# Optimization experiments

Measured on AMD Instinct MI355X. Metric: run time of the kernel, lower is better.

The kernel has to match this reference:

```python
import jax, jax.numpy as jnp
import numpy as np

D_MODEL = 1024
N_HEADS = 16
D_K = D_MODEL // N_HEADS
D_FF = 4096
LN_EPS = 1e-5


def _layer_norm(x, gamma, beta):
    mu = jnp.mean(x, axis=-1, keepdims=True)
    var = jnp.mean(jnp.square(x - mu), axis=-1, keepdims=True)
    return (x - mu) * jax.lax.rsqrt(var + LN_EPS) * gamma + beta


def setup_inputs() -> dict:
    key = jax.random.key(0)
    ks = jax.random.split(key, 16)
    B, S = 2, 2048
    x = jax.random.normal(ks[0], (B, S, D_MODEL), dtype=jnp.float32)
    # causal mask: True = masked (as used by masked_fill)
    mask = ~jnp.tril(jnp.ones((S, S), dtype=bool))
    s = 1.0 / np.sqrt(D_MODEL)
    sf = 1.0 / np.sqrt(D_FF)
    inp = {
        "x": x,
        "mask": mask,
        "ln1_g": jnp.ones((D_MODEL,), jnp.float32),
        "ln1_b": jnp.zeros((D_MODEL,), jnp.float32),
        "ln2_g": jnp.ones((D_MODEL,), jnp.float32),
        "ln2_b": jnp.zeros((D_MODEL,), jnp.float32),
        "Wq": jax.random.normal(ks[1], (D_MODEL, D_MODEL), jnp.float32) * s,
        "bq": jax.random.normal(ks[2], (D_MODEL,), jnp.float32) * s,
        "Wk": jax.random.normal(ks[3], (D_MODEL, D_MODEL), jnp.float32) * s,
        "bk": jax.random.normal(ks[4], (D_MODEL,), jnp.float32) * s,
        "Wv": jax.random.normal(ks[5], (D_MODEL, D_MODEL), jnp.float32) * s,
        "bv": jax.random.normal(ks[6], (D_MODEL,), jnp.float32) * s,
        "Wo": jax.random.normal(ks[7], (D_MODEL, D_MODEL), jnp.float32) * s,
        "bo": jax.random.normal(ks[8], (D_MODEL,), jnp.float32) * s,
        "W1": jax.random.normal(ks[9], (D_MODEL, D_FF), jnp.float32) * s,
        "b1": jax.random.normal(ks[10], (D_FF,), jnp.float32) * s,
        "W2": jax.random.normal(ks[11], (D_FF, D_MODEL), jnp.float32) * sf,
        "b2": jax.random.normal(ks[12], (D_MODEL,), jnp.float32) * sf,
    }
    return inp


def reference(x, mask, ln1_g, ln1_b, ln2_g, ln2_b,
              Wq, bq, Wk, bk, Wv, bv, Wo, bo, W1, b1, W2, b2):
    B, S, _ = x.shape
    normed = _layer_norm(x, ln1_g, ln1_b)
    # project and split heads: [B, H, S, Dk]
    def split_heads(t):
        return t.reshape(B, S, N_HEADS, D_K).transpose(0, 2, 1, 3)
    Q = split_heads(normed @ Wq + bq)
    K = split_heads(normed @ Wk + bk)
    V = split_heads(normed @ Wv + bv)
    qk = jnp.einsum("bhsd,bhtd->bhst", Q, K)  # [B, H, S, S]
    qk = jnp.where(mask, -jnp.inf, qk)  # mask applied BEFORE scaling, as in source
    attn = jax.nn.softmax(qk / np.sqrt(D_K), axis=-1)
    attn_out = jnp.einsum("bhst,bhtd->bhsd", attn, V)
    attn_out = attn_out.transpose(0, 2, 1, 3).reshape(B, S, D_MODEL)
    attn_out = attn_out @ Wo + bo
    res = attn_out + x  # dropout_p=0 (eval)
    h = _layer_norm(res, ln2_g, ln2_b)
    h = jax.nn.gelu(h @ W1 + b1, approximate=False)
    h = h @ W2 + b2
    return res + h
```

## Files before the change

kernel.cpp:

```cpp
#include <hip/hip_runtime.h>


typedef __bf16 bf16;
typedef __bf16 bf16x4 __attribute__((ext_vector_type(4)));
typedef __bf16 bf16x8 __attribute__((ext_vector_type(8)));
typedef float f32x4 __attribute__((ext_vector_type(4)));

#define NROWS 4096
#define DM 1024
#define SEQ 2048
#define NHEAD 16
#define DKH 64
#define DFF 4096
#define QSCALE 0.18033688f

#define GLL16(gptr, lptr) \
  __builtin_amdgcn_global_load_lds((const __attribute__((address_space(1))) void*)(gptr), \
                                   (__attribute__((address_space(3))) void*)(lptr), 16, 0, 0)

static char* g_scratch = nullptr;
namespace {
struct ScratchInit {
  ScratchInit() {
    void* p = nullptr;
    if (hipMalloc(&p, (size_t)128 * 1024 * 1024) == hipSuccess) g_scratch = (char*)p;
  }
};
static ScratchInit g_scratch_init;
}

__device__ inline unsigned cvt_pk_bf16(float lo, float hi) {
  unsigned r;
  asm("v_cvt_pk_bf16_f32 %0, %1, %2" : "=v"(r) : "v"(lo), "v"(hi));
  return r;
}

__global__ __launch_bounds__(256) void ln_kernel(const float* __restrict__ inp,
                                                 const float* __restrict__ gamma,
                                                 const float* __restrict__ beta,
                                                 bf16* __restrict__ out) {
  int row = blockIdx.x;
  int t = threadIdx.x;
  float4 xv = *((const float4*)(inp + (size_t)row * DM) + t);
  float v[4] = {xv.x, xv.y, xv.z, xv.w};
  float s = 0.f, sq = 0.f;
#pragma unroll
  for (int i = 0; i < 4; i++) { s += v[i]; sq += v[i] * v[i]; }
#pragma unroll
  for (int m = 32; m >= 1; m >>= 1) { s += __shfl_xor(s, m); sq += __shfl_xor(sq, m); }
  __shared__ float rs[4], rq[4];
  int w = t >> 6, lane = t & 63;
  if (lane == 0) { rs[w] = s; rq[w] = sq; }
  __syncthreads();
  s = rs[0] + rs[1] + rs[2] + rs[3];
  sq = rq[0] + rq[1] + rq[2] + rq[3];
  float mu = s * (1.f / DM);
  float var = sq * (1.f / DM) - mu * mu;
  float rinv = rsqrtf(var + 1e-5f);
  float4 gv = *((const float4*)gamma + t);
  float4 bv = *((const float4*)beta + t);
  float g[4] = {gv.x, gv.y, gv.z, gv.w}, b[4] = {bv.x, bv.y, bv.z, bv.w};
  bf16 ov[4];
#pragma unroll
  for (int i = 0; i < 4; i++) ov[i] = (bf16)((v[i] - mu) * rinv * g[i] + b[i]);
  *(uint2*)(out + (size_t)row * DM + t * 4) = *(uint2*)ov;
}

__global__ __launch_bounds__(256) void concat_bias(const float* __restrict__ bq,
                                                   const float* __restrict__ bk,
                                                   const float* __restrict__ bv,
                                                   float* __restrict__ cat) {
  int i = blockIdx.x * 256 + threadIdx.x;
  float v = (i < 1024) ? bq[i] : (i < 2048 ? bk[i - 1024] : bv[i - 2048]);
  cat[i] = v;
}

__global__ __launch_bounds__(1024) void transpose_f32_bf16(const float* __restrict__ in,
                                                           bf16* __restrict__ out,
                                                           int R, int C) {
  __shared__ bf16 tile[32][33];
  int x = blockIdx.x * 32 + threadIdx.x;
  int y = blockIdx.y * 32 + threadIdx.y;
  tile[threadIdx.y][threadIdx.x] = (bf16)in[(size_t)y * C + x];
  __syncthreads();
  int ox = blockIdx.y * 32 + threadIdx.x;
  int oy = blockIdx.x * 32 + threadIdx.y;
  out[(size_t)oy * R + ox] = tile[threadIdx.x][threadIdx.y];
}

__global__ __launch_bounds__(1024) void transpose_bf16(const bf16* __restrict__ in,
                                                       bf16* __restrict__ out,
                                                       int R, int C) {
  __shared__ bf16 tile[32][33];
  size_t zoff = (size_t)blockIdx.z * (size_t)R * (size_t)C;
  int x = blockIdx.x * 32 + threadIdx.x;
  int y = blockIdx.y * 32 + threadIdx.y;
  tile[threadIdx.y][threadIdx.x] = in[zoff + (size_t)y * C + x];
  __syncthreads();
  int ox = blockIdx.y * 32 + threadIdx.x;
  int oy = blockIdx.x * 32 + threadIdx.y;
  out[zoff + (size_t)oy * R + ox] = tile[threadIdx.x][threadIdx.y];
}

#define BM 128
#define BK 64

#define EPI_QKV3 0
#define EPI_ATTN_RES 1
#define EPI_GELU 2
#define EPI_FFN2 3

template<int EPI, int BNT>
__global__ __launch_bounds__(256, 2) void gemm_bt(
    const bf16* __restrict__ A, const bf16* __restrict__ Bt,
    const float* __restrict__ bias, int Kd, int N,
    bf16* __restrict__ outb, float* __restrict__ outf,
    const float* __restrict__ add) {
  constexpr int MS = (BNT == 128) ? 4 : 2;
  __shared__ bf16 As[BM * BK];
  __shared__ bf16 Bs[BNT * BK];
  int t = threadIdx.x;
  int m0 = blockIdx.y * BM, n0 = blockIdx.x * BNT;
  int w = t >> 6, lane = t & 63, ln = lane & 15, quad = lane >> 4;
  int wm = (BNT == 128) ? (w >> 1) * 64 : w * 32;
  int wn = (BNT == 128) ? (w & 1) * 64 : 0;
  f32x4 acc[MS][4];
#pragma unroll
  for (int i = 0; i < MS; i++)
#pragma unroll
    for (int j = 0; j < 4; j++) acc[i][j] = (f32x4){0.f, 0.f, 0.f, 0.f};

  int lr = (t >> 3) & 7, lc = t & 7;
  int gcol = ((lc ^ lr) * 8);
  const bf16* Ab = A + (size_t)(m0 + w * 8 + lr) * Kd + gcol;
  const bf16* Bb = Bt + (size_t)(n0 + w * 8 + lr) * Kd + gcol;
  bf16* AsW = As + (w * 8) * BK;
  bf16* BsW = Bs + (w * 8) * BK;

  for (int k0 = 0; k0 < Kd; k0 += BK) {
    __syncthreads();
#pragma unroll
    for (int j = 0; j < 4; j++)
      GLL16(Ab + (size_t)(32 * j) * Kd + k0, AsW + 32 * j * BK);
#pragma unroll
    for (int j = 0; j < BNT / 32; j++)
      GLL16(Bb + (size_t)(32 * j) * Kd + k0, BsW + 32 * j * BK);
    __syncthreads();
#pragma unroll
    for (int kk = 0; kk < 2; kk++) {
      bf16x8 af[MS], bfr[4];
#pragma unroll
      for (int ms = 0; ms < MS; ms++) {
        int r = wm + ms * 16 + ln;
        af[ms] = *(const bf16x8*)(As + r * BK + (((kk * 4 + quad) ^ (r & 7)) * 8));
      }
#pragma unroll
      for (int ns = 0; ns < 4; ns++) {
        int r = wn + ns * 16 + ln;
        bfr[ns] = *(const bf16x8*)(Bs + r * BK + (((kk * 4 + quad) ^ (r & 7)) * 8));
      }
#pragma unroll
      for (int ms = 0; ms < MS; ms++)
#pragma unroll
        for (int ns = 0; ns < 4; ns++)
          acc[ms][ns] = __builtin_amdgcn_mfma_f32_16x16x32_bf16(af[ms], bfr[ns], acc[ms][ns], 0, 0, 0);
    }
  }

#pragma unroll
  for (int ms = 0; ms < MS; ms++) {
#pragma unroll
    for (int ns = 0; ns < 4; ns++) {
      int col = n0 + wn + ns * 16 + ln;
      float bv = bias[col];
#pragma unroll
      for (int r = 0; r < 4; r++) {
        int row = m0 + wm + ms * 16 + quad * 4 + r;
        float val = acc[ms][ns][r] + bv;
        if (EPI == EPI_QKV3) {
          int which = col >> 10, cc = col & 1023;
          int h = cc >> 6, dk = cc & 63;
          float sc = (which == 0) ? QSCALE : 1.f;
          int b = row >> 11, sx = row & 2047;
          outb[(size_t)which * (4 << 20) +
               ((((size_t)b * NHEAD + h) * SEQ) + sx) * DKH + dk] = (bf16)(val * sc);
        } else if (EPI == EPI_ATTN_RES) {
          size_t idx = (size_t)row * DM + col;
          outf[idx] = val + add[idx];
        } else if (EPI == EPI_GELU) {
          float gl = 0.5f * val * (1.f + erff(val * 0.7071067811865475f));
          outb[(size_t)row * N + col] = (bf16)gl;
        } else {
          size_t idx = (size_t)row * DM + col;
          outf[idx] = val + add[idx];
        }
      }
    }
  }
}

#define OSTR 68

__global__ __launch_bounds__(256) void attn_kernel(
    const bf16* __restrict__ Q, const bf16* __restrict__ K,
    const bf16* __restrict__ Vt, bf16* __restrict__ out) {
  __shared__ float smem[2 * 32 * OSTR + 128];
  int lin = blockIdx.x;
  int bh = lin & 31;
  int qq = 63 - (lin >> 5);
  int t = threadIdx.x, w = t >> 6, lane = t & 63, ln = lane & 15, quad = lane >> 4;
  int qbase = qq * 32;
  size_t bhS = (size_t)bh * SEQ;
  const bf16* Vg0 = Vt + (size_t)bh * DKH * SEQ;

  bf16x8 qa[2][2];
#pragma unroll
  for (int m = 0; m < 2; m++)
#pragma unroll
    for (int ks = 0; ks < 2; ks++)
      qa[m][ks] = *(const bf16x8*)(Q + (bhS + qbase + m * 16 + ln) * DKH + ks * 32 + quad * 8);

  bf16x8 ones;
#pragma unroll
  for (int i = 0; i < 8; i++) ones[i] = (bf16)1.0f;

  f32x4 o[2][4];
#pragma unroll
  for (int m = 0; m < 2; m++)
#pragma unroll
    for (int i = 0; i < 4; i++) o[m][i] = (f32x4){0.f, 0.f, 0.f, 0.f};
  f32x4 accl[2] = {(f32x4){0.f, 0.f, 0.f, 0.f}, (f32x4){0.f, 0.f, 0.f, 0.f}};

  int ktmax = qq >> 1;
  for (int kt = w; kt <= ktmax; kt += 4) {
    const bf16* Kg = K + (bhS + kt * 64) * DKH;
    bf16x8 kbf[8], vbf[8];
#pragma unroll
    for (int ns = 0; ns < 4; ns++)
#pragma unroll
      for (int ks = 0; ks < 2; ks++)
        kbf[ns * 2 + ks] = *(const bf16x8*)(Kg + (ns * 16 + ln) * DKH + ks * 32 + quad * 8);
#pragma unroll
    for (int ns = 0; ns < 4; ns++)
#pragma unroll
      for (int j = 0; j < 2; j++) {
        const bf16* vrow = Vg0 + (size_t)(ns * 16 + ln) * SEQ + kt * 64 + j * 32 + quad * 4;
        union { bf16x8 v; bf16x4 h[2]; } tmp;
        tmp.h[0] = *(const bf16x4*)(vrow);
        tmp.h[1] = *(const bf16x4*)(vrow + 16);
        vbf[ns * 2 + j] = tmp.v;
      }

    f32x4 s[2][4];
#pragma unroll
    for (int m = 0; m < 2; m++)
#pragma unroll
      for (int ns = 0; ns < 4; ns++) s[m][ns] = (f32x4){0.f, 0.f, 0.f, 0.f};
#pragma unroll
    for (int ns = 0; ns < 4; ns++)
#pragma unroll
      for (int m = 0; m < 2; m++) {
        s[m][ns] = __builtin_amdgcn_mfma_f32_16x16x32_bf16(kbf[ns * 2], qa[m][0], s[m][ns], 0, 0, 0);
        s[m][ns] = __builtin_amdgcn_mfma_f32_16x16x32_bf16(kbf[ns * 2 + 1], qa[m][1], s[m][ns], 0, 0, 0);
      }
    if (kt == ktmax) {
#pragma unroll
      for (int m = 0; m < 2; m++)
#pragma unroll
        for (int ns = 0; ns < 4; ns++)
#pragma unroll
          for (int r = 0; r < 4; r++) {
            int qrow = qbase + m * 16 + ln;
            int kpos = kt * 64 + ns * 16 + quad * 4 + r;
            if (kpos > qrow) s[m][ns][r] = -30000.f;
          }
    }
#pragma unroll
    for (int m = 0; m < 2; m++)
#pragma unroll
      for (int ns = 0; ns < 4; ns++)
#pragma unroll
        for (int r = 0; r < 4; r++)
          s[m][ns][r] = __builtin_amdgcn_exp2f(s[m][ns][r]);
    bf16x8 pa[2][2];
#pragma unroll
    for (int m = 0; m < 2; m++)
#pragma unroll
      for (int j = 0; j < 2; j++) {
        union { bf16x8 v; unsigned u[4]; } pk;
        pk.u[0] = cvt_pk_bf16(s[m][2 * j][0], s[m][2 * j][1]);
        pk.u[1] = cvt_pk_bf16(s[m][2 * j][2], s[m][2 * j][3]);
        pk.u[2] = cvt_pk_bf16(s[m][2 * j + 1][0], s[m][2 * j + 1][1]);
        pk.u[3] = cvt_pk_bf16(s[m][2 * j + 1][2], s[m][2 * j + 1][3]);
        pa[m][j] = pk.v;
      }
#pragma unroll
    for (int m = 0; m < 2; m++) {
      accl[m] = __builtin_amdgcn_mfma_f32_16x16x32_bf16(pa[m][0], ones, accl[m], 0, 0, 0);
      accl[m] = __builtin_amdgcn_mfma_f32_16x16x32_bf16(pa[m][1], ones, accl[m], 0, 0, 0);
    }
#pragma unroll
    for (int ns2 = 0; ns2 < 4; ns2++)
#pragma unroll
      for (int m = 0; m < 2; m++) {
        o[m][ns2] = __builtin_amdgcn_mfma_f32_16x16x32_bf16(pa[m][0], vbf[ns2 * 2], o[m][ns2], 0, 0, 0);
        o[m][ns2] = __builtin_amdgcn_mfma_f32_16x16x32_bf16(pa[m][1], vbf[ns2 * 2 + 1], o[m][ns2], 0, 0, 0);
      }
  }

  float* Ob = smem;
  float* Lb = smem + 2 * 32 * OSTR;
#pragma unroll
  for (int m = 0; m < 2; m++) {
    if (w < 2) {
#pragma unroll
      for (int ns2 = 0; ns2 < 4; ns2++)
#pragma unroll
        for (int r = 0; r < 4; r++)
          Ob[(w * 32 + m * 16 + quad * 4 + r) * OSTR + ns2 * 16 + ln] = o[m][ns2][r];
    }
    if (ln == 0) {
#pragma unroll
      for (int r = 0; r < 4; r++) Lb[w * 32 + m * 16 + quad * 4 + r] = accl[m][r];
    }
  }
  __syncthreads();
  if (w >= 2) {
#pragma unroll
    for (int m = 0; m < 2; m++)
#pragma unroll
      for (int ns2 = 0; ns2 < 4; ns2++)
#pragma unroll
        for (int r = 0; r < 4; r++) {
          int idx = ((w - 2) * 32 + m * 16 + quad * 4 + r) * OSTR + ns2 * 16 + ln;
          Ob[idx] += o[m][ns2][r];
        }
  }
  __syncthreads();

  int r = t >> 3, c0 = (t & 7) * 8;
  float l = Lb[r] + Lb[32 + r] + Lb[64 + r] + Lb[96 + r];
  float inv = 1.f / l;
  bf16 ov[8];
#pragma unroll
  for (int j = 0; j < 8; j++) {
    float v = Ob[r * OSTR + c0 + j] + Ob[(32 + r) * OSTR + c0 + j];
    ov[j] = (bf16)(v * inv);
  }
  int b = bh >> 4, h = bh & 15;
  *(uint4*)(out + ((size_t)b * SEQ + qbase + r) * DM + h * DKH + c0) = *(uint4*)ov;
}

extern "C" void kernel_launch(void* const* d_in, const int* in_sizes, int n_in,
                              void* d_out, int out_size, void* d_ws, size_t ws_size,
                              hipStream_t stream) {
  const float* x    = (const float*)d_in[0];
  const float* ln1g = (const float*)d_in[2];
  const float* ln1b = (const float*)d_in[3];
  const float* ln2g = (const float*)d_in[4];
  const float* ln2b = (const float*)d_in[5];
  const float* Wq = (const float*)d_in[6];   const float* bq = (const float*)d_in[7];
  const float* Wk = (const float*)d_in[8];   const float* bk = (const float*)d_in[9];
  const float* Wv = (const float*)d_in[10];  const float* bv = (const float*)d_in[11];
  const float* Wo = (const float*)d_in[12];  const float* bo = (const float*)d_in[13];
  const float* W1 = (const float*)d_in[14];  const float* b1 = (const float*)d_in[15];
  const float* W2 = (const float*)d_in[16];  const float* b2 = (const float*)d_in[17];
  float* outp = (float*)d_out;

  char* scratch = g_scratch ? g_scratch : (char*)d_ws;

  bf16* Wqt = (bf16*)scratch;
  bf16* Wkt = Wqt + (1 << 20);
  bf16* Wvt = Wkt + (1 << 20);
  bf16* Wot = Wvt + (1 << 20);
  bf16* W1t = Wot + (1 << 20);
  bf16* W2t = W1t + (4 << 20);
  bf16* normed = W2t + (4 << 20);
  bf16* Qb = normed + (4 << 20);
  bf16* Kb = Qb + (4 << 20);
  bf16* Vb = Kb + (4 << 20);
  bf16* Vtb = Vb + (4 << 20);
  bf16* attn_o = Vtb + (4 << 20);
  float* resf = (float*)(attn_o + (4 << 20));
  float* bias_cat = resf + (4 << 20);
  bf16* h1 = Qb;

  dim3 b256(256), b1k(32, 32);

  ln_kernel<<<NROWS, b256, 0, stream>>>(x, ln1g, ln1b, normed);
  concat_bias<<<12, b256, 0, stream>>>(bq, bk, bv, bias_cat);

  transpose_f32_bf16<<<dim3(32, 32), b1k, 0, stream>>>(Wq, Wqt, 1024, 1024);
  transpose_f32_bf16<<<dim3(32, 32), b1k, 0, stream>>>(Wk, Wkt, 1024, 1024);
  transpose_f32_bf16<<<dim3(32, 32), b1k, 0, stream>>>(Wv, Wvt, 1024, 1024);
  transpose_f32_bf16<<<dim3(32, 32), b1k, 0, stream>>>(Wo, Wot, 1024, 1024);
  transpose_f32_bf16<<<dim3(128, 32), b1k, 0, stream>>>(W1, W1t, 1024, 4096);
  transpose_f32_bf16<<<dim3(32, 128), b1k, 0, stream>>>(W2, W2t, 4096, 1024);

  gemm_bt<EPI_QKV3, 128><<<dim3(24, 32), b256, 0, stream>>>(
      normed, Wqt, bias_cat, 1024, 3072, Qb, nullptr, nullptr);

  transpose_bf16<<<dim3(2, 64, 32), b1k, 0, stream>>>(Vb, Vtb, 2048, 64);

  attn_kernel<<<dim3(2048), b256, 0, stream>>>(Qb, Kb, Vtb, attn_o);

  gemm_bt<EPI_ATTN_RES, 64><<<dim3(16, 32), b256, 0, stream>>>(
      attn_o, Wot, bo, 1024, 1024, nullptr, resf, x);

  ln_kernel<<<NROWS, b256, 0, stream>>>(resf, ln2g, ln2b, normed);

  gemm_bt<EPI_GELU, 128><<<dim3(32, 32), b256, 0, stream>>>(
      normed, W1t, b1, 1024, 4096, h1, nullptr, nullptr);

  gemm_bt<EPI_FFN2, 64><<<dim3(16, 32), b256, 0, stream>>>(
      h1, W2t, b2, 4096, 1024, nullptr, outp, resf);
}
```

Before: 426.5 us.

## Prefetch next K tile in attention loop and permute V transpose for 16-byte loads

The attention loop is restructured to double-buffer K fragments in registers, loading the next K tile while computing the current one. Separately, the V transpose kernel writes columns in a permuted order so each lane can fetch its V fragment with one 16-byte load instead of two 8-byte loads. This targets global load latency and instruction count in the attention kernel. The cost is higher register pressure, which could lower occupancy.

```diff
diff --git a/kernel.cpp b/kernel.cpp
--- a/kernel.cpp
+++ b/kernel.cpp
@@ -2,7 +2,6 @@
 
 
 typedef __bf16 bf16;
-typedef __bf16 bf16x4 __attribute__((ext_vector_type(4)));
 typedef __bf16 bf16x8 __attribute__((ext_vector_type(8)));
 typedef float f32x4 __attribute__((ext_vector_type(4)));
 
@@ -88,9 +87,9 @@
   out[(size_t)oy * R + ox] = tile[threadIdx.x][threadIdx.y];
 }
 
-__global__ __launch_bounds__(1024) void transpose_bf16(const bf16* __restrict__ in,
-                                                       bf16* __restrict__ out,
-                                                       int R, int C) {
+__global__ __launch_bounds__(1024) void transpose_bf16_vperm(const bf16* __restrict__ in,
+                                                             bf16* __restrict__ out,
+                                                             int R, int C) {
   __shared__ bf16 tile[32][33];
   size_t zoff = (size_t)blockIdx.z * (size_t)R * (size_t)C;
   int x = blockIdx.x * 32 + threadIdx.x;
@@ -99,7 +98,8 @@
   __syncthreads();
   int ox = blockIdx.y * 32 + threadIdx.x;
   int oy = blockIdx.x * 32 + threadIdx.y;
-  out[zoff + (size_t)oy * R + ox] = tile[threadIdx.x][threadIdx.y];
+  int oxp = (ox & ~31) | (((ox >> 2) & 3) << 3) | (((ox >> 4) & 1) << 2) | (ox & 3);
+  out[zoff + (size_t)oy * R + oxp] = tile[threadIdx.x][threadIdx.y];
 }
 
 #define BM 128
@@ -232,25 +232,23 @@
   f32x4 accl[2] = {(f32x4){0.f, 0.f, 0.f, 0.f}, (f32x4){0.f, 0.f, 0.f, 0.f}};
 
   int ktmax = qq >> 1;
-  for (int kt = w; kt <= ktmax; kt += 4) {
-    const bf16* Kg = K + (bhS + kt * 64) * DKH;
-    bf16x8 kbf[8], vbf[8];
+
+  auto LOADK = [&](bf16x8 (&kf)[8], int kt_) {
+    const bf16* Kg = K + (bhS + kt_ * 64) * DKH;
 #pragma unroll
     for (int ns = 0; ns < 4; ns++)
 #pragma unroll
       for (int ks = 0; ks < 2; ks++)
-        kbf[ns * 2 + ks] = *(const bf16x8*)(Kg + (ns * 16 + ln) * DKH + ks * 32 + quad * 8);
+        kf[ns * 2 + ks] = *(const bf16x8*)(Kg + (ns * 16 + ln) * DKH + ks * 32 + quad * 8);
+  };
+  auto LOADV = [&](bf16x8 (&vf)[8], int kt_) {
 #pragma unroll
     for (int ns = 0; ns < 4; ns++)
 #pragma unroll
-      for (int j = 0; j < 2; j++) {
-        const bf16* vrow = Vg0 + (size_t)(ns * 16 + ln) * SEQ + kt * 64 + j * 32 + quad * 4;
-        union { bf16x8 v; bf16x4 h[2]; } tmp;
-        tmp.h[0] = *(const bf16x4*)(vrow);
-        tmp.h[1] = *(const bf16x4*)(vrow + 16);
-        vbf[ns * 2 + j] = tmp.v;
-      }
-
+      for (int ks = 0; ks < 2; ks++)
+        vf[ns * 2 + ks] = *(const bf16x8*)(Vg0 + (size_t)(ns * 16 + ln) * SEQ + kt_ * 64 + ks * 32 + quad * 8);
+  };
+  auto COMPUTE = [&](bf16x8 (&kf)[8], bf16x8 (&vf)[8], int kt_) {
     f32x4 s[2][4];
 #pragma unroll
     for (int m = 0; m < 2; m++)
@@ -260,10 +258,10 @@
     for (int ns = 0; ns < 4; ns++)
 #pragma unroll
       for (int m = 0; m < 2; m++) {
-        s[m][ns] = __builtin_amdgcn_mfma_f32_16x16x32_bf16(kbf[ns * 2], qa[m][0], s[m][ns], 0, 0, 0);
-        s[m][ns] = __builtin_amdgcn_mfma_f32_16x16x32_bf16(kbf[ns * 2 + 1], qa[m][1], s[m][ns], 0, 0, 0);
-      }
-    if (kt == ktmax) {
+        s[m][ns] = __builtin_amdgcn_mfma_f32_16x16x32_bf16(kf[ns * 2], qa[m][0], s[m][ns], 0, 0, 0);
+        s[m][ns] = __builtin_amdgcn_mfma_f32_16x16x32_bf16(kf[ns * 2 + 1], qa[m][1], s[m][ns], 0, 0, 0);
+      }
+    if (kt_ == ktmax) {
 #pragma unroll
       for (int m = 0; m < 2; m++)
 #pragma unroll
@@ -271,7 +269,7 @@
 #pragma unroll
           for (int r = 0; r < 4; r++) {
             int qrow = qbase + m * 16 + ln;
-            int kpos = kt * 64 + ns * 16 + quad * 4 + r;
+            int kpos = kt_ * 64 + ns * 16 + quad * 4 + r;
             if (kpos > qrow) s[m][ns][r] = -30000.f;
           }
     }
@@ -303,9 +301,37 @@
     for (int ns2 = 0; ns2 < 4; ns2++)
 #pragma unroll
       for (int m = 0; m < 2; m++) {
-        o[m][ns2] = __builtin_amdgcn_mfma_f32_16x16x32_bf16(pa[m][0], vbf[ns2 * 2], o[m][ns2], 0, 0, 0);
-        o[m][ns2] = __builtin_amdgcn_mfma_f32_16x16x32_bf16(pa[m][1], vbf[ns2 * 2 + 1], o[m][ns2], 0, 0, 0);
-      }
+        o[m][ns2] = __builtin_amdgcn_mfma_f32_16x16x32_bf16(pa[m][0], vf[ns2 * 2], o[m][ns2], 0, 0, 0);
+        o[m][ns2] = __builtin_amdgcn_mfma_f32_16x16x32_bf16(pa[m][1], vf[ns2 * 2 + 1], o[m][ns2], 0, 0, 0);
+      }
+  };
+
+  int kt = w;
+  if (kt <= ktmax) {
+    bf16x8 ka[8], kb[8];
+    LOADK(ka, kt);
+    while (true) {
+      {
+        bf16x8 vf[8];
+        LOADV(vf, kt);
+        int ktn = kt + 4;
+        bool more = ktn <= ktmax;
+        if (more) LOADK(kb, ktn);
+        COMPUTE(ka, vf, kt);
+        if (!more) break;
+        kt = ktn;
+      }
+      {
+        bf16x8 vf[8];
+        LOADV(vf, kt);
+        int ktn = kt + 4;
+        bool more = ktn <= ktmax;
+        if (more) LOADK(ka, ktn);
+        COMPUTE(kb, vf, kt);
+        if (!more) break;
+        kt = ktn;
+      }
+    }
   }
 
   float* Ob = smem;
@@ -400,7 +426,7 @@
   gemm_bt<EPI_QKV3, 128><<<dim3(24, 32), b256, 0, stream>>>(
       normed, Wqt, bias_cat, 1024, 3072, Qb, nullptr, nullptr);
 
-  transpose_bf16<<<dim3(2, 64, 32), b1k, 0, stream>>>(Vb, Vtb, 2048, 64);
+  transpose_bf16_vperm<<<dim3(2, 64, 32), b1k, 0, stream>>>(Vb, Vtb, 2048, 64);
 
   attn_kernel<<<dim3(2048), b256, 0, stream>>>(Qb, Kb, Vtb, attn_o);
 
```

Result: faster. 413.9 us (-3.0%).
